# Performance work log

Measured on AMD Instinct MI355X. Metric: run time of the kernel, lower is better.

The kernel has to match this reference:

```python
import jax, jax.numpy as jnp
import numpy as np

N = 100000
E = 3200000
F_IN = 128
H = 16
NUM_GRAPHS = 1000


def gcn_conv(x, W, b, src, dst, norm, n_nodes):
    # x: [N, Fin] -> h: [N, Fout]; gather along src, scale, scatter-add to dst
    h = x @ W
    msg = h[src] * norm[:, None]            # [E_tot, Fout]
    out = jax.ops.segment_sum(msg, dst, num_segments=n_nodes)
    return out + b


def setup_inputs() -> dict:
    key = jax.random.key(0)
    k0, k1, k2, k3, k4, k5 = jax.random.split(key, 6)
    x = jax.random.normal(k0, (N, F_IN), dtype=jnp.float32)
    edge_index = jax.random.randint(k1, (2, E), 0, N, dtype=jnp.int64)
    batch = jnp.sort(jax.random.randint(k2, (N,), 0, NUM_GRAPHS, dtype=jnp.int64))
    # Glorot-style init for GCN weights, zero bias (PyG default)
    W1 = jax.random.normal(k3, (F_IN, H), dtype=jnp.float32) / np.sqrt(F_IN)
    b1 = jnp.zeros((H,), dtype=jnp.float32)
    W2 = jax.random.normal(k4, (H, 1), dtype=jnp.float32) / np.sqrt(H)
    b2 = jnp.zeros((1,), dtype=jnp.float32)
    return {"x": x, "edge_index": edge_index, "batch": batch,
            "W1": W1, "b1": b1, "W2": W2, "b2": b2}


def reference(x, edge_index, batch, W1, b1, W2, b2):
    n_nodes = x.shape[0]
    # add self-loops (PyG GCNConv default)
    loop = jnp.arange(n_nodes, dtype=edge_index.dtype)
    src = jnp.concatenate([edge_index[0], loop])
    dst = jnp.concatenate([edge_index[1], loop])
    # symmetric normalization D^{-1/2} (A+I) D^{-1/2}
    deg = jax.ops.segment_sum(jnp.ones_like(dst, dtype=x.dtype), dst,
                              num_segments=n_nodes)
    dinv = jnp.where(deg > 0, jax.lax.rsqrt(deg), 0.0)
    norm = dinv[src] * dinv[dst]            # [E_tot]

    h = gcn_conv(x, W1, b1, src, dst, norm, n_nodes)   # [N, 16]
    h = jax.nn.relu(h)
    h = gcn_conv(h, W2, b2, src, dst, norm, n_nodes)   # [N, 1]
    # global_add_pool over graphs
    out = jax.ops.segment_sum(h, batch, num_segments=NUM_GRAPHS)  # [G, 1]
    return out
```

## Files before the change

kernel.cpp:

```cpp
#include <hip/hip_runtime.h>

#define NB_MAX   512
#define CHUNK    8192
#define CAPB     16384
#define SORT_CAP 12288

__device__ inline unsigned short f2bf(float f) {
    unsigned u = __float_as_uint(f);
    u += 0x7FFFu + ((u >> 16) & 1u);
    return (unsigned short)(u >> 16);
}

__global__ void k_zero(float* __restrict__ out, int g, int* __restrict__ bcnt) {
    int t = blockIdx.x * blockDim.x + threadIdx.x;
    if (t < g) out[t] = 0.f;
    if (t < NB_MAX) bcnt[t] = 0;
}

__global__ __launch_bounds__(512) void k_scatter(const int* __restrict__ src,
                                                 const int* __restrict__ dst,
                                                 int* __restrict__ bcnt,
                                                 int* __restrict__ packed,
                                                 int E) {
    __shared__ int lh[NB_MAX];
    __shared__ int ldelta[NB_MAX];
    __shared__ int wsum[8];
    __shared__ int sorted[CHUNK];
    __shared__ unsigned short sbkt[CHUNK];
    int t = threadIdx.x;
    int e0 = blockIdx.x * CHUNK;
    int e1 = min(e0 + CHUNK, E);
    int cnt = e1 - e0;
    lh[t] = 0;
    __syncthreads();
    for (int e = e0 + t; e < e1; e += 512) atomicAdd(&lh[dst[e] >> 8], 1);
    __syncthreads();
    int v = lh[t];
    int lane = t & 63, wid = t >> 6;
    int s = v;
#pragma unroll
    for (int o = 1; o < 64; o <<= 1) {
        int u = __shfl_up(s, o, 64);
        if (lane >= o) s += u;
    }
    if (lane == 63) wsum[wid] = s;
    __syncthreads();
    int base = 0;
#pragma unroll
    for (int w = 0; w < 8; w++) base += (w < wid) ? wsum[w] : 0;
    int ex = s + base - v;
    int gbase = v ? atomicAdd(&bcnt[t], v) : 0;
    lh[t] = ex;
    ldelta[t] = t * CAPB + gbase - ex;
    __syncthreads();
    for (int e = e0 + t; e < e1; e += 512) {
        int d = dst[e];
        int b = d >> 8;
        int r = atomicAdd(&lh[b], 1);
        sorted[r] = src[e] | ((d & 255) << 24);
        sbkt[r] = (unsigned short)b;
    }
    __syncthreads();
    for (int i = t; i < cnt; i += 512)
        packed[i + ldelta[sbkt[i]]] = sorted[i];
}

__global__ __launch_bounds__(512) void k_sortgemm(const int* __restrict__ packed,
                                                  const int* __restrict__ bcnt,
                                                  const float* __restrict__ x,
                                                  const float* __restrict__ W1,
                                                  int* __restrict__ sidx2,
                                                  int* __restrict__ noffs,
                                                  int* __restrict__ ndeg,
                                                  float* __restrict__ dinv,
                                                  unsigned short* __restrict__ hs,
                                                  int n) {
    __shared__ int hist[256];
    __shared__ int curs[256];
    __shared__ int wsum[4];
    __shared__ float sdinv[256];
    __shared__ float sW[128 * 16];
    __shared__ __align__(16) char smem[SORT_CAP * 4];
    int* sorted = (int*)smem;
    float* sXT = (float*)smem;

    int t = threadIdx.x, b = blockIdx.x;
    int seg0 = b * CAPB, cnt = bcnt[b];
    int node0 = b << 8;

    for (int q = t; q < 2048; q += 512) sW[q] = W1[q];
    if (t < 256) hist[t] = 0;
    __syncthreads();
    for (int e = t; e < cnt; e += 512)
        atomicAdd(&hist[(unsigned)packed[seg0 + e] >> 24], 1);
    __syncthreads();
    int v = 0, s = 0;
    if (t < 256) { v = hist[t]; s = v; }
    int lane = t & 63, wid = t >> 6;
#pragma unroll
    for (int o = 1; o < 64; o <<= 1) {
        int u = __shfl_up(s, o, 64);
        if (lane >= o) s += u;
    }
    if (t < 256 && lane == 63) wsum[wid] = s;
    __syncthreads();
    int ex = 0;
    if (t < 256) {
        int base = 0;
#pragma unroll
        for (int w = 0; w < 4; w++) base += (w < wid) ? wsum[w] : 0;
        ex = s + base - v;
        float di = rsqrtf((float)v + 1.0f);
        sdinv[t] = di;
        int node = node0 + t;
        if (node < n) {
            noffs[node] = seg0 + ex;
            ndeg[node] = v;
            dinv[node] = di;
        }
    }
    if (cnt <= SORT_CAP) {
        if (t < 256) curs[t] = ex;
        __syncthreads();
        for (int e = t; e < cnt; e += 512) {
            int p = packed[seg0 + e];
            int dl = (int)((unsigned)p >> 24);
            int r = atomicAdd(&curs[dl], 1);
            sorted[r] = p & 0xFFFFFF;
        }
        __syncthreads();
        for (int i = t; i < cnt; i += 512)
            sidx2[seg0 + i] = sorted[i];
    } else {
        if (t < 256) curs[t] = seg0 + ex;
        __syncthreads();
        for (int e = t; e < cnt; e += 512) {
            int p = packed[seg0 + e];
            int dl = (int)((unsigned)p >> 24);
            int r = atomicAdd(&curs[dl], 1);
            sidx2[r] = p & 0xFFFFFF;
        }
    }

    int ng = t >> 2, cg = t & 3;
    float acc[2][4];
#pragma unroll
    for (int i = 0; i < 2; i++)
#pragma unroll
        for (int j = 0; j < 4; j++) acc[i][j] = 0.f;
    for (int kc = 0; kc < 4; kc++) {
        __syncthreads();
#pragma unroll
        for (int pass = 0; pass < 4; pass++) {
            int row = pass * 64 + (t >> 3);
            int node = node0 + row;
            const float* xp = x + (size_t)min(node, n - 1) * 128 + kc * 32 + (t & 7) * 4;
            float4 vv = *(const float4*)xp;
            int k0 = (t & 7) * 4;
            sXT[(k0 + 0) * 260 + row] = vv.x;
            sXT[(k0 + 1) * 260 + row] = vv.y;
            sXT[(k0 + 2) * 260 + row] = vv.z;
            sXT[(k0 + 3) * 260 + row] = vv.w;
        }
        __syncthreads();
        const float* wbase = sW + kc * 32 * 16 + cg * 4;
#pragma unroll 8
        for (int k = 0; k < 32; k++) {
            float2 xv = *(const float2*)&sXT[k * 260 + ng * 2];
            float4 wv = *(const float4*)&wbase[k * 16];
            acc[0][0] += xv.x * wv.x; acc[0][1] += xv.x * wv.y;
            acc[0][2] += xv.x * wv.z; acc[0][3] += xv.x * wv.w;
            acc[1][0] += xv.y * wv.x; acc[1][1] += xv.y * wv.y;
            acc[1][2] += xv.y * wv.z; acc[1][3] += xv.y * wv.w;
        }
    }
#pragma unroll
    for (int i = 0; i < 2; i++) {
        int local = ng * 2 + i;
        int node = node0 + local;
        if (node < n) {
            float di = sdinv[local];
            ushort4 o;
            o.x = f2bf(acc[i][0] * di);
            o.y = f2bf(acc[i][1] * di);
            o.z = f2bf(acc[i][2] * di);
            o.w = f2bf(acc[i][3] * di);
            *(ushort4*)&hs[(size_t)node * 16 + cg * 4] = o;
        }
    }
}

#define UNPACK_ADD2(u)                                       \
    acc[0] += __uint_as_float((u).x << 16);                  \
    acc[1] += __uint_as_float((u).x & 0xFFFF0000u);          \
    acc[2] += __uint_as_float((u).y << 16);                  \
    acc[3] += __uint_as_float((u).y & 0xFFFF0000u);

__global__ __launch_bounds__(256) void k_agg1(const uint2* __restrict__ hs2,
                                              const int* __restrict__ noffs,
                                              const int* __restrict__ ndeg,
                                              const int* __restrict__ sidx2,
                                              const float* __restrict__ dinv,
                                              const float* __restrict__ b1,
                                              const float* __restrict__ W2,
                                              float* __restrict__ hw, int n) {
    int tid = blockIdx.x * 256 + threadIdx.x;
    int node = tid >> 2, q = tid & 3;
    if (node >= n) return;
    float acc[4];
    uint2 u0 = hs2[(size_t)node * 4 + q];
    acc[0] = __uint_as_float(u0.x << 16);
    acc[1] = __uint_as_float(u0.x & 0xFFFF0000u);
    acc[2] = __uint_as_float(u0.y << 16);
    acc[3] = __uint_as_float(u0.y & 0xFFFF0000u);
    int e0 = noffs[node], e1 = e0 + ndeg[node];
    int e = e0;
    for (; e + 7 < e1; e += 8) {
        int s0 = sidx2[e],     s1 = sidx2[e + 1];
        int s2 = sidx2[e + 2], s3 = sidx2[e + 3];
        int s4 = sidx2[e + 4], s5 = sidx2[e + 5];
        int s6 = sidx2[e + 6], s7 = sidx2[e + 7];
        uint2 a0 = hs2[(size_t)s0 * 4 + q];
        uint2 a1 = hs2[(size_t)s1 * 4 + q];
        uint2 a2 = hs2[(size_t)s2 * 4 + q];
        uint2 a3 = hs2[(size_t)s3 * 4 + q];
        uint2 a4 = hs2[(size_t)s4 * 4 + q];
        uint2 a5 = hs2[(size_t)s5 * 4 + q];
        uint2 a6 = hs2[(size_t)s6 * 4 + q];
        uint2 a7 = hs2[(size_t)s7 * 4 + q];
        UNPACK_ADD2(a0) UNPACK_ADD2(a1) UNPACK_ADD2(a2) UNPACK_ADD2(a3)
        UNPACK_ADD2(a4) UNPACK_ADD2(a5) UNPACK_ADD2(a6) UNPACK_ADD2(a7)
    }
    for (; e < e1; e++) {
        uint2 a = hs2[(size_t)sidx2[e] * 4 + q];
        UNPACK_ADD2(a)
    }
    float di = dinv[node];
    int base = q * 4;
    float r = 0.f;
#pragma unroll
    for (int j = 0; j < 4; j++)
        r += fmaxf(di * acc[j] + b1[base + j], 0.f) * W2[base + j];
    r += __shfl_down(r, 2, 4);
    r += __shfl_down(r, 1, 4);
    if (q == 0) hw[node] = r * di;
}

__global__ __launch_bounds__(256) void k_agg2(const float* __restrict__ hw,
                                              const int* __restrict__ noffs,
                                              const int* __restrict__ ndeg,
                                              const int* __restrict__ sidx2,
                                              const float* __restrict__ dinv,
                                              const float* __restrict__ b2,
                                              const int* __restrict__ batch,
                                              float* __restrict__ out, int n) {
    __shared__ float v[128];
    __shared__ int g[128];
    int t = threadIdx.x;
    int tid = blockIdx.x * 256 + t;
    int i = tid >> 1, q = tid & 1;
    int li = t >> 1;
    float acc = 0.f;
    int gid = -1;
    if (i < n) {
        if (q == 0) acc = hw[i];
        int e0 = noffs[i], e1 = e0 + ndeg[i];
        int e = e0 + q;
        for (; e + 6 < e1; e += 8)
            acc += hw[sidx2[e]] + hw[sidx2[e + 2]] + hw[sidx2[e + 4]] + hw[sidx2[e + 6]];
        for (; e < e1; e += 2) acc += hw[sidx2[e]];
    }
    acc += __shfl_down(acc, 1, 2);
    if (q == 0) {
        if (i < n) {
            v[li] = dinv[i] * acc + b2[0];
            g[li] = batch[i];
        } else {
            v[li] = 0.f;
            g[li] = -1;
        }
    }
    __syncthreads();
    if (q == 0) {
        int gid2 = g[li];
        if (gid2 >= 0 && (li == 0 || g[li - 1] != gid2)) {
            float sum = v[li];
            for (int w = li + 1; w < 128 && g[w] == gid2; w++) sum += v[w];
            atomicAdd(&out[gid2], sum);
        }
    }
}

extern "C" void kernel_launch(void* const* d_in, const int* in_sizes, int n_in,
                              void* d_out, int out_size, void* d_ws, size_t ws_size,
                              hipStream_t stream) {
    int n = in_sizes[0] / 128;
    int E = in_sizes[1] / 2;
    const float* x     = (const float*)d_in[0];
    const int*   ei    = (const int*)d_in[1];
    const int*   src   = ei;
    const int*   dst   = ei + E;
    const int*   batch = (const int*)d_in[2];
    const float* W1    = (const float*)d_in[3];
    const float* b1    = (const float*)d_in[4];
    const float* W2    = (const float*)d_in[5];
    const float* b2    = (const float*)d_in[6];
    float* out = (float*)d_out;

    int nb = (n + 255) >> 8;

    char* p = (char*)d_ws;
    auto carve = [&](size_t bytes) {
        void* r = (void*)p;
        p += (bytes + 63) & ~(size_t)63;
        return r;
    };
    int*            bcnt   = (int*)carve(NB_MAX * 4);
    int*            packed = (int*)carve((size_t)nb * CAPB * 4);
    int*            sidx2  = (int*)carve((size_t)nb * CAPB * 4);
    int*            noffs  = (int*)carve((size_t)n * 4);
    int*            ndeg   = (int*)carve((size_t)n * 4);
    float*          dinv   = (float*)carve((size_t)n * 4);
    unsigned short* hs     = (unsigned short*)carve((size_t)n * 16 * 2);
    float*          hw     = (float*)carve((size_t)n * 4);

    k_zero<<<(out_size + 1023) / 1024, 1024, 0, stream>>>(out, out_size, bcnt);
    k_scatter<<<(E + CHUNK - 1) / CHUNK, 512, 0, stream>>>(src, dst, bcnt, packed, E);
    k_sortgemm<<<nb, 512, 0, stream>>>(packed, bcnt, x, W1, sidx2, noffs, ndeg,
                                       dinv, hs, n);
    k_agg1<<<((size_t)n * 4 + 255) / 256, 256, 0, stream>>>((const uint2*)hs, noffs, ndeg,
                                                            sidx2, dinv, b1, W2, hw, n);
    k_agg2<<<((size_t)n * 2 + 255) / 256, 256, 0, stream>>>(hw, noffs, ndeg, sidx2,
                                                            dinv, b2, batch, out, n);
}
```

Measured before the change: 118.5 us.

## Cache edge loads in registers and prefetch x tiles ahead of GEMM

The scatter kernel now loads src/dst once into 16 registers per thread during the histogram pass and reuses them in the placement pass, so the second global read is gone. The sort+GEMM kernel likewise keeps the first 8192 packed entries in registers between the histogram and placement passes, and loads the first x tile before the sort phase. It then prefetches each following x chunk into registers while the current chunk is written to shared memory, overlapping global latency with compute. This costs extra register pressure, which may lower occupancy.

Measured after the change: 114.6 us, median of 2. 3.3% less time.

```diff
diff --git a/kernel.cpp b/kernel.cpp
--- a/kernel.cpp
+++ b/kernel.cpp
@@ -33,7 +33,18 @@
     int cnt = e1 - e0;
     lh[t] = 0;
     __syncthreads();
-    for (int e = e0 + t; e < e1; e += 512) atomicAdd(&lh[dst[e] >> 8], 1);
+    int pv[16], bv[16];
+#pragma unroll
+    for (int j = 0; j < 16; j++) {
+        int e = e0 + t + j * 512;
+        bool ok = e < e1;
+        int d = ok ? dst[e] : 0;
+        int sv = ok ? src[e] : 0;
+        int b = d >> 8;
+        pv[j] = sv | ((d & 255) << 24);
+        bv[j] = ok ? b : -1;
+        if (ok) atomicAdd(&lh[b], 1);
+    }
     __syncthreads();
     int v = lh[t];
     int lane = t & 63, wid = t >> 6;
@@ -53,12 +64,14 @@
     lh[t] = ex;
     ldelta[t] = t * CAPB + gbase - ex;
     __syncthreads();
-    for (int e = e0 + t; e < e1; e += 512) {
-        int d = dst[e];
-        int b = d >> 8;
-        int r = atomicAdd(&lh[b], 1);
-        sorted[r] = src[e] | ((d & 255) << 24);
-        sbkt[r] = (unsigned short)b;
+#pragma unroll
+    for (int j = 0; j < 16; j++) {
+        int b = bv[j];
+        if (b >= 0) {
+            int r = atomicAdd(&lh[b], 1);
+            sorted[r] = pv[j];
+            sbkt[r] = (unsigned short)b;
+        }
     }
     __syncthreads();
     for (int i = t; i < cnt; i += 512)
@@ -88,10 +101,27 @@
     int seg0 = b * CAPB, cnt = bcnt[b];
     int node0 = b << 8;
 
+    float4 xreg[4];
+#pragma unroll
+    for (int pass = 0; pass < 4; pass++) {
+        int row = pass * 64 + (t >> 3);
+        int node = node0 + row;
+        xreg[pass] = *(const float4*)(x + (size_t)min(node, n - 1) * 128 + (t & 7) * 4);
+    }
+
     for (int q = t; q < 2048; q += 512) sW[q] = W1[q];
     if (t < 256) hist[t] = 0;
     __syncthreads();
-    for (int e = t; e < cnt; e += 512)
+    int pv[16];
+#pragma unroll
+    for (int j = 0; j < 16; j++) {
+        int e = t + j * 512;
+        bool ok = e < cnt;
+        int p = ok ? packed[seg0 + e] : 0;
+        pv[j] = p;
+        if (ok) atomicAdd(&hist[(unsigned)p >> 24], 1);
+    }
+    for (int e = CHUNK + t; e < cnt; e += 512)
         atomicAdd(&hist[(unsigned)packed[seg0 + e] >> 24], 1);
     __syncthreads();
     int v = 0, s = 0;
@@ -122,10 +152,18 @@
     if (cnt <= SORT_CAP) {
         if (t < 256) curs[t] = ex;
         __syncthreads();
-        for (int e = t; e < cnt; e += 512) {
+#pragma unroll
+        for (int j = 0; j < 16; j++) {
+            int e = t + j * 512;
+            if (e < cnt) {
+                int p = pv[j];
+                int r = atomicAdd(&curs[(unsigned)p >> 24], 1);
+                sorted[r] = p & 0xFFFFFF;
+            }
+        }
+        for (int e = CHUNK + t; e < cnt; e += 512) {
             int p = packed[seg0 + e];
-            int dl = (int)((unsigned)p >> 24);
-            int r = atomicAdd(&curs[dl], 1);
+            int r = atomicAdd(&curs[(unsigned)p >> 24], 1);
             sorted[r] = p & 0xFFFFFF;
         }
         __syncthreads();
@@ -153,14 +191,20 @@
 #pragma unroll
         for (int pass = 0; pass < 4; pass++) {
             int row = pass * 64 + (t >> 3);
-            int node = node0 + row;
-            const float* xp = x + (size_t)min(node, n - 1) * 128 + kc * 32 + (t & 7) * 4;
-            float4 vv = *(const float4*)xp;
             int k0 = (t & 7) * 4;
-            sXT[(k0 + 0) * 260 + row] = vv.x;
-            sXT[(k0 + 1) * 260 + row] = vv.y;
-            sXT[(k0 + 2) * 260 + row] = vv.z;
-            sXT[(k0 + 3) * 260 + row] = vv.w;
+            sXT[(k0 + 0) * 260 + row] = xreg[pass].x;
+            sXT[(k0 + 1) * 260 + row] = xreg[pass].y;
+            sXT[(k0 + 2) * 260 + row] = xreg[pass].z;
+            sXT[(k0 + 3) * 260 + row] = xreg[pass].w;
+        }
+        if (kc < 3) {
+#pragma unroll
+            for (int pass = 0; pass < 4; pass++) {
+                int row = pass * 64 + (t >> 3);
+                int node = node0 + row;
+                xreg[pass] = *(const float4*)(x + (size_t)min(node, n - 1) * 128
+                                              + (kc + 1) * 32 + (t & 7) * 4);
+            }
         }
         __syncthreads();
         const float* wbase = sW + kc * 32 * 16 + cg * 4;
```
